# Optimization experiments

Measured on AMD Instinct MI355X. Metric: run time of the kernel, lower is better.

## Reference

```python
import jax, jax.numpy as jnp
import numpy as np

HIDDEN = 128
N_LAYERS = 6
N_NODES = 50000
N_EDGES = 640000


def _glorot(key, shape):
    fan_in, fan_out = shape[0], shape[1]
    lim = (6.0 / (fan_in + fan_out)) ** 0.5
    return jax.random.uniform(key, shape, jnp.float32, -lim, lim)


def setup_inputs() -> dict:
    key = jax.random.key(0)
    ks = jax.random.split(key, 8)
    pos = jax.random.normal(ks[0], (N_NODES, 3), jnp.float32)
    edge_attr = jax.random.normal(ks[1], (N_EDGES, 3), jnp.float32)
    edge_index = jax.random.randint(ks[2], (2, N_EDGES), 0, N_NODES, jnp.int64)
    enc_w = _glorot(ks[3], (3, HIDDEN)); enc_b = jnp.zeros((HIDDEN,), jnp.float32)
    dec_w = _glorot(ks[4], (HIDDEN, 3)); dec_b = jnp.zeros((3,), jnp.float32)
    lk = jax.random.split(ks[5], 4 * N_LAYERS)
    edge_w1 = jnp.stack([_glorot(lk[4 * i + 0], (3 * HIDDEN, HIDDEN)) for i in range(N_LAYERS)])
    edge_w2 = jnp.stack([_glorot(lk[4 * i + 1], (HIDDEN, HIDDEN)) for i in range(N_LAYERS)])
    node_w1 = jnp.stack([_glorot(lk[4 * i + 2], (2 * HIDDEN, HIDDEN)) for i in range(N_LAYERS)])
    node_w2 = jnp.stack([_glorot(lk[4 * i + 3], (HIDDEN, HIDDEN)) for i in range(N_LAYERS)])
    edge_b1 = jnp.zeros((N_LAYERS, HIDDEN), jnp.float32)
    edge_b2 = jnp.zeros((N_LAYERS, HIDDEN), jnp.float32)
    node_b1 = jnp.zeros((N_LAYERS, HIDDEN), jnp.float32)
    node_b2 = jnp.zeros((N_LAYERS, HIDDEN), jnp.float32)
    return dict(pos=pos, edge_attr=edge_attr, edge_index=edge_index,
                enc_w=enc_w, enc_b=enc_b, dec_w=dec_w, dec_b=dec_b,
                edge_w1=edge_w1, edge_b1=edge_b1, edge_w2=edge_w2, edge_b2=edge_b2,
                node_w1=node_w1, node_b1=node_b1, node_w2=node_w2, node_b2=node_b2)


def _interaction(x, ef, src, dst, ew1, eb1, ew2, eb2, nw1, nb1, nw2, nb2, n_nodes):
    # message: concat(x_i=x[dst], x_j=x[src], edge_feature) -> edge MLP
    m = jnp.concatenate([x[dst], x[src], ef], axis=-1)            # [E, 3H]
    m = jax.nn.relu(m @ ew1 + eb1) @ ew2 + eb2                     # [E, H]
    # scatter-mean by target node
    sums = jax.ops.segment_sum(m, dst, num_segments=n_nodes)      # [N, H]
    cnt = jax.ops.segment_sum(jnp.ones((m.shape[0],), m.dtype), dst, num_segments=n_nodes)
    aggr = sums / jnp.maximum(cnt, 1.0)[:, None]
    node = jnp.concatenate([x, aggr], axis=-1)                     # [N, 2H]
    node = jax.nn.relu(node @ nw1 + nb1) @ nw2 + nb2               # [N, H]
    return x + node, ef + m


def reference(pos, edge_attr, edge_index, enc_w, enc_b, dec_w, dec_b,
              edge_w1, edge_b1, edge_w2, edge_b2,
              node_w1, node_b1, node_w2, node_b2):
    n_nodes = pos.shape[0]
    src = edge_index[0]
    dst = edge_index[1]
    x = jnp.zeros((n_nodes, HIDDEN), jnp.float32)
    ef = edge_attr @ enc_w + enc_b
    for i in range(N_LAYERS):
        x, ef = _interaction(x, ef, src, dst,
                             edge_w1[i], edge_b1[i], edge_w2[i], edge_b2[i],
                             node_w1[i], node_b1[i], node_w2[i], node_b2[i], n_nodes)
    out = x @ dec_w + dec_b                                        # [N, 3]
    # F.normalize(dim=1, eps=1e-12)
    norm = jnp.linalg.norm(out, axis=1, keepdims=True)
    return out / jnp.maximum(norm, 1e-12)
```

## Files before the change

### kernel.cpp

```cpp
#include <hip/hip_runtime.h>
#include <cstdint>

#define HIDDEN  128
#define NLAYERS 6
#define NNODES  50000
#define NEDGES  640000

typedef short short8 __attribute__((ext_vector_type(8)));
typedef float f32x4  __attribute__((ext_vector_type(4)));

__device__ __forceinline__ float bf2f(unsigned short u) {
    return __uint_as_float(((unsigned int)u) << 16);
}
__device__ __forceinline__ unsigned short f2bf(float f) {
    unsigned int u = __float_as_uint(f);
    unsigned int r = u + 0x7FFFu + ((u >> 16) & 1u);
    return (unsigned short)(r >> 16);
}
__device__ __forceinline__ unsigned int pack2(float a, float b) {
    return (unsigned int)f2bf(a) | ((unsigned int)f2bf(b) << 16);
}
__device__ __forceinline__ void unpack8(uint4 v, float* f) {
    f[0] = bf2f((unsigned short)(v.x & 0xffff)); f[1] = bf2f((unsigned short)(v.x >> 16));
    f[2] = bf2f((unsigned short)(v.y & 0xffff)); f[3] = bf2f((unsigned short)(v.y >> 16));
    f[4] = bf2f((unsigned short)(v.z & 0xffff)); f[5] = bf2f((unsigned short)(v.z >> 16));
    f[6] = bf2f((unsigned short)(v.w & 0xffff)); f[7] = bf2f((unsigned short)(v.w >> 16));
}

__global__ void detect_kernel(const int* __restrict__ ei, int* __restrict__ flag)
{
    int lane = threadIdx.x;
    int v = ei[2 * lane + 1];
    unsigned long long b = __ballot(v != 0);
    if (lane == 0) *flag = (b != 0ULL) ? 1 : 0;
}

__global__ void normidx_kernel(const int* __restrict__ ei, const int* __restrict__ flag,
                               int* __restrict__ s32, int* __restrict__ d32)
{
    int e = blockIdx.x * blockDim.x + threadIdx.x;
    if (e >= NEDGES) return;
    int s, d;
    if (*flag) { s = ei[e]; d = ei[NEDGES + e]; }
    else       { s = ei[2 * e]; d = ei[2 * (NEDGES + e)]; }
    s32[e] = min(max(s, 0), NNODES - 1);
    d32[e] = min(max(d, 0), NNODES - 1);
}

__global__ void degree_kernel(const int* __restrict__ dst, int* __restrict__ deg)
{
    int e = blockIdx.x * blockDim.x + threadIdx.x;
    if (e < NEDGES) atomicAdd(&deg[dst[e]], 1);
}

#define SCAN_T 1024
__global__ void scan_kernel(const int* __restrict__ deg, int* __restrict__ off,
                            int* __restrict__ cursor)
{
    __shared__ int part[SCAN_T];
    const int t = threadIdx.x;
    const int CH = (NNODES + SCAN_T - 1) / SCAN_T;
    const int base = t * CH;
    int s = 0;
    for (int i = 0; i < CH; ++i) {
        int idx = base + i;
        if (idx < NNODES) s += deg[idx];
    }
    part[t] = s;
    __syncthreads();
    for (int d = 1; d < SCAN_T; d <<= 1) {
        int v = (t >= d) ? part[t - d] : 0;
        __syncthreads();
        part[t] += v;
        __syncthreads();
    }
    int run = (t == 0) ? 0 : part[t - 1];
    for (int i = 0; i < CH; ++i) {
        int idx = base + i;
        if (idx < NNODES) {
            off[idx] = run;
            cursor[idx] = run;
            run += deg[idx];
        }
    }
    if (t == SCAN_T - 1) off[NNODES] = run;
}

__global__ void scatter_kernel(const int* __restrict__ s32, const int* __restrict__ d32,
                               int* __restrict__ cursor,
                               int* __restrict__ sp, int* __restrict__ dp, int* __restrict__ ep)
{
    int e = blockIdx.x * blockDim.x + threadIdx.x;
    if (e >= NEDGES) return;
    int d = d32[e];
    int p = atomicAdd(&cursor[d], 1);
    sp[p] = s32[e];
    dp[p] = d;
    ep[p] = e;
}

__global__ void transpose_kernel(const float* __restrict__ W, unsigned short* __restrict__ WT,
                                 int K, int N, int L)
{
    long idx = (long)blockIdx.x * 256 + threadIdx.x;
    long tot = (long)L * K * N;
    if (idx >= tot) return;
    int kn = (int)(idx % ((long)K * N));
    int l  = (int)(idx / ((long)K * N));
    int k = kn / N;
    int n = kn % N;
    WT[(long)l * K * N + (long)n * K + k] = f2bf(W[idx]);
}

__global__ void encode_kernel(const float* __restrict__ ea,
                              const float* __restrict__ w,
                              const float* __restrict__ b,
                              const int* __restrict__ ep,
                              unsigned short* __restrict__ ef)
{
    int idx = blockIdx.x * blockDim.x + threadIdx.x;
    int p = idx >> 5;
    if (p >= NEDGES) return;
    int e = ep[p];
    int j = (idx & 31) << 2;
    float a0 = ea[e * 3 + 0], a1 = ea[e * 3 + 1], a2 = ea[e * 3 + 2];
    float4 w0 = *(const float4*)(w + 0 * HIDDEN + j);
    float4 w1 = *(const float4*)(w + 1 * HIDDEN + j);
    float4 w2 = *(const float4*)(w + 2 * HIDDEN + j);
    float4 bb = *(const float4*)(b + j);
    ushort4 o;
    o.x = f2bf(fmaf(a0, w0.x, fmaf(a1, w1.x, fmaf(a2, w2.x, bb.x))));
    o.y = f2bf(fmaf(a0, w0.y, fmaf(a1, w1.y, fmaf(a2, w2.y, bb.y))));
    o.z = f2bf(fmaf(a0, w0.z, fmaf(a1, w1.z, fmaf(a2, w2.z, bb.z))));
    o.w = f2bf(fmaf(a0, w0.w, fmaf(a1, w1.w, fmaf(a2, w2.w, bb.w))));
    *(ushort4*)(ef + (long)p * HIDDEN + j) = o;
}

__global__ __launch_bounds__(256, 3)
void edge_layer_mfma(const unsigned short* __restrict__ Xa,
                     const unsigned short* __restrict__ Xb,
                     unsigned short* __restrict__ ef,
                     float* __restrict__ sums,
                     const int* __restrict__ sp,
                     const int* __restrict__ dp,
                     const unsigned short* __restrict__ W1T,
                     const float* __restrict__ b1,
                     const unsigned short* __restrict__ W2T,
                     const float* __restrict__ b2)
{
    __shared__ __align__(16) unsigned char buf[45056];
    unsigned short* As = (unsigned short*)buf;
    unsigned short* Hs = (unsigned short*)buf;
    unsigned short* Bs = (unsigned short*)(buf + 34816);
    __shared__ int dv[128];
    __shared__ int sv[128];

    const int tid = threadIdx.x;
    const long eb = (long)blockIdx.x * 128;
    if (tid < 128) dv[tid]       = dp[eb + tid];
    else           sv[tid - 128] = sp[eb + tid - 128];

    const int lane = tid & 63;
    const int wv   = tid >> 6;
    const int mn   = lane & 15;
    const int q    = lane >> 4;
    const int rr   = tid >> 1;
    const int o    = (tid & 1) << 4;
    const int bn   = tid >> 1;
    const int bk   = (tid & 1) << 4;

    f32x4 acc[2][8];
#pragma unroll
    for (int h = 0; h < 2; ++h)
#pragma unroll
        for (int t = 0; t < 8; ++t) acc[h][t] = (f32x4)0.0f;

    short8 efold0[4], efold1[4];

    uint4 pa0, pa1, pw0, pw1;
    {
        const unsigned short* epp = ef + (eb + rr) * HIDDEN + o;
        pa0 = *(const uint4*)epp;
        pa1 = *(const uint4*)(epp + 8);
        const unsigned short* wp = W1T + (long)bn * 384 + 256 + bk;
        pw0 = *(const uint4*)wp;
        pw1 = *(const uint4*)(wp + 8);
    }

    for (int c = 0; c < 4; ++c) {
        *(uint4*)&As[rr * 40 + o]      = pa0;
        *(uint4*)&As[rr * 40 + o + 8]  = pa1;
        *(uint4*)&Bs[bn * 40 + bk]     = pw0;
        *(uint4*)&Bs[bn * 40 + bk + 8] = pw1;
        __syncthreads();

        if (c + 1 < 4) {
            const int cn = c + 1;
            const unsigned short* epp = ef + (eb + rr) * HIDDEN + (cn << 5) + o;
            pa0 = *(const uint4*)epp;
            pa1 = *(const uint4*)(epp + 8);
            const unsigned short* wp = W1T + (long)bn * 384 + 256 + (cn << 5) + bk;
            pw0 = *(const uint4*)wp;
            pw1 = *(const uint4*)(wp + 8);
        }

        short8 af0 = *(short8*)&As[(wv * 32 + mn) * 40 + (q << 3)];
        short8 af1 = *(short8*)&As[(wv * 32 + 16 + mn) * 40 + (q << 3)];
        efold0[c] = af0;
        efold1[c] = af1;
#pragma unroll
        for (int nt = 0; nt < 8; ++nt) {
            short8 bf = *(short8*)&Bs[(nt * 16 + mn) * 40 + (q << 3)];
            acc[0][nt] = __builtin_amdgcn_mfma_f32_16x16x32_bf16(af0, bf, acc[0][nt], 0, 0, 0);
            acc[1][nt] = __builtin_amdgcn_mfma_f32_16x16x32_bf16(af1, bf, acc[1][nt], 0, 0, 0);
        }
        __syncthreads();
    }

#pragma unroll
    for (int h = 0; h < 2; ++h)
#pragma unroll
        for (int nt = 0; nt < 8; ++nt)
#pragma unroll
            for (int r = 0; r < 4; ++r)
                Hs[(wv * 32 + h * 16 + q * 4 + r) * 136 + nt * 16 + mn] = f2bf(acc[h][nt][r]);

    {
        const int row  = wv * 32 + (lane >> 1);
        const int ch   = (lane & 1) << 6;
        const unsigned short* xap = Xa + (long)dv[row] * HIDDEN + ch;
        const unsigned short* xbp = Xb + (long)sv[row] * HIDDEN + ch;
        unsigned short* hp = &Hs[row * 136 + ch];
#pragma unroll
        for (int i = 0; i < 8; ++i) {
            uint4 va = *(const uint4*)(xap + (i << 3));
            uint4 vb = *(const uint4*)(xbp + (i << 3));
            uint4 vp = *(uint4*)(hp + (i << 3));
            float fa[8], fb[8], fp[8];
            unpack8(va, fa); unpack8(vb, fb); unpack8(vp, fp);
            const float* bp = b1 + ch + (i << 3);
            uint4 nw;
            float h0 = fmaxf(fp[0] + fa[0] + fb[0] + bp[0], 0.0f);
            float h1 = fmaxf(fp[1] + fa[1] + fb[1] + bp[1], 0.0f);
            float h2 = fmaxf(fp[2] + fa[2] + fb[2] + bp[2], 0.0f);
            float h3 = fmaxf(fp[3] + fa[3] + fb[3] + bp[3], 0.0f);
            float h4 = fmaxf(fp[4] + fa[4] + fb[4] + bp[4], 0.0f);
            float h5 = fmaxf(fp[5] + fa[5] + fb[5] + bp[5], 0.0f);
            float h6 = fmaxf(fp[6] + fa[6] + fb[6] + bp[6], 0.0f);
            float h7 = fmaxf(fp[7] + fa[7] + fb[7] + bp[7], 0.0f);
            nw.x = pack2(h0, h1); nw.y = pack2(h2, h3);
            nw.z = pack2(h4, h5); nw.w = pack2(h6, h7);
            *(uint4*)(hp + (i << 3)) = nw;
        }
    }

    f32x4 acc2[2][8];
#pragma unroll
    for (int h = 0; h < 2; ++h)
#pragma unroll
        for (int t = 0; t < 8; ++t) acc2[h][t] = (f32x4)0.0f;
    {
        const unsigned short* wp = W2T + (long)bn * 128 + bk;
        pw0 = *(const uint4*)wp;
        pw1 = *(const uint4*)(wp + 8);
    }
    for (int c = 0; c < 4; ++c) {
        *(uint4*)&Bs[bn * 40 + bk]     = pw0;
        *(uint4*)&Bs[bn * 40 + bk + 8] = pw1;
        __syncthreads();
        if (c + 1 < 4) {
            const unsigned short* wp = W2T + (long)bn * 128 + ((c + 1) << 5) + bk;
            pw0 = *(const uint4*)wp;
            pw1 = *(const uint4*)(wp + 8);
        }
        short8 af0 = *(short8*)&Hs[(wv * 32 + mn) * 136 + (c << 5) + (q << 3)];
        short8 af1 = *(short8*)&Hs[(wv * 32 + 16 + mn) * 136 + (c << 5) + (q << 3)];
#pragma unroll
        for (int nt = 0; nt < 8; ++nt) {
            short8 bf = *(short8*)&Bs[(nt * 16 + mn) * 40 + (q << 3)];
            acc2[0][nt] = __builtin_amdgcn_mfma_f32_16x16x32_bf16(af0, bf, acc2[0][nt], 0, 0, 0);
            acc2[1][nt] = __builtin_amdgcn_mfma_f32_16x16x32_bf16(af1, bf, acc2[1][nt], 0, 0, 0);
        }
        __syncthreads();
    }

#pragma unroll
    for (int h = 0; h < 2; ++h)
#pragma unroll
        for (int nt = 0; nt < 8; ++nt) {
            float b2v = b2[nt * 16 + mn];
#pragma unroll
            for (int r = 0; r < 4; ++r)
                Hs[(wv * 32 + h * 16 + q * 4 + r) * 136 + nt * 16 + mn] = f2bf(acc2[h][nt][r] + b2v);
        }

#pragma unroll
    for (int h = 0; h < 2; ++h) {
        const int row = wv * 32 + h * 16 + mn;
        unsigned short* ep_ = ef + (eb + row) * HIDDEN + (q << 3);
#pragma unroll
        for (int c = 0; c < 4; ++c) {
            uint4 mh = *(uint4*)&Hs[row * 136 + (c << 5) + (q << 3)];
            float m[8], e[8];
            unpack8(mh, m);
            short8 eo = h ? efold1[c] : efold0[c];
            uint4 eu = *(uint4*)&eo;
            unpack8(eu, e);
            uint4 nw;
            nw.x = pack2(e[0] + m[0], e[1] + m[1]);
            nw.y = pack2(e[2] + m[2], e[3] + m[3]);
            nw.z = pack2(e[4] + m[4], e[5] + m[5]);
            nw.w = pack2(e[6] + m[6], e[7] + m[7]);
            *(uint4*)(ep_ + (c << 5)) = nw;
        }
    }

    {
        const int cp = (tid & 63) << 1;
        const int qr = tid >> 6;
        float s0 = 0.0f, s1 = 0.0f;
        int cur = dv[qr * 32];
        for (int r = 0; r < 32; ++r) {
            const int row = qr * 32 + r;
            const int d = dv[row];
            if (d != cur) {
                atomicAdd(&sums[(long)cur * HIDDEN + cp], s0);
                atomicAdd(&sums[(long)cur * HIDDEN + cp + 1], s1);
                s0 = 0.0f; s1 = 0.0f;
                cur = d;
            }
            unsigned int u = *(unsigned int*)&Hs[row * 136 + cp];
            s0 += bf2f((unsigned short)(u & 0xffff));
            s1 += bf2f((unsigned short)(u >> 16));
        }
        atomicAdd(&sums[(long)cur * HIDDEN + cp], s0);
        atomicAdd(&sums[(long)cur * HIDDEN + cp + 1], s1);
    }
}

__global__ __launch_bounds__(256, 5)
void node_layer_mfma(float* __restrict__ x,
                     float* __restrict__ sums,
                     const int* __restrict__ deg,
                     const unsigned short* __restrict__ N1T,
                     const float* __restrict__ b1,
                     const unsigned short* __restrict__ N2T,
                     const float* __restrict__ b2,
                     const unsigned short* __restrict__ W1Tn,
                     unsigned short* __restrict__ Xa,
                     unsigned short* __restrict__ Xb)
{
    __shared__ __align__(16) unsigned char nbuf[27648];
    unsigned short* As = (unsigned short*)nbuf;
    unsigned short* Hs = (unsigned short*)nbuf;
    unsigned short* Bs = (unsigned short*)(nbuf + 17408);
    __shared__ float cInv[64];

    const int tid = threadIdx.x;
    const long n0 = (long)blockIdx.x * 64;
    if (tid < 64) {
        long n = n0 + tid;
        cInv[tid] = (n < NNODES) ? 1.0f / fmaxf((float)deg[n], 1.0f) : 0.0f;
    }

    const int lane = tid & 63;
    const int wv   = tid >> 6;
    const int mn   = lane & 15;
    const int q    = lane >> 4;
    const int srow = tid >> 2;
    const int sseg = tid & 3;
    const int bn   = tid >> 1;
    const int bk   = (tid & 1) << 4;

    long nr = n0 + srow;
    if (nr >= NNODES) nr = NNODES - 1;

    __syncthreads();

    f32x4 acc[8];
#pragma unroll
    for (int t = 0; t < 8; ++t) acc[t] = (f32x4)0.0f;

    float4 pa0, pa1;
    uint4 pb0, pb1;
    {
        const float* spx = x + nr * HIDDEN + (sseg << 3);
        pa0 = *(const float4*)spx;
        pa1 = *(const float4*)(spx + 4);
        const unsigned short* wp = N1T + (long)bn * 256 + bk;
        pb0 = *(const uint4*)wp;
        pb1 = *(const uint4*)(wp + 8);
    }
    float scCur = 1.0f;
    for (int c = 0; c < 8; ++c) {
        {
            uint4 w;
            w.x = pack2(pa0.x * scCur, pa0.y * scCur); w.y = pack2(pa0.z * scCur, pa0.w * scCur);
            w.z = pack2(pa1.x * scCur, pa1.y * scCur); w.w = pack2(pa1.z * scCur, pa1.w * scCur);
            *(uint4*)&As[srow * 40 + (sseg << 3)] = w;
        }
        *(uint4*)&Bs[bn * 40 + bk]     = pb0;
        *(uint4*)&Bs[bn * 40 + bk + 8] = pb1;
        __syncthreads();
        if (c + 1 < 8) {
            const int cn = c + 1;
            const float* base = (cn < 4) ? x : sums;
            scCur = (cn < 4) ? 1.0f : cInv[srow];
            const float* spx = base + nr * HIDDEN + ((cn & 3) << 5) + (sseg << 3);
            pa0 = *(const float4*)spx;
            pa1 = *(const float4*)(spx + 4);
            const unsigned short* wp = N1T + (long)bn * 256 + (cn << 5) + bk;
            pb0 = *(const uint4*)wp;
            pb1 = *(const uint4*)(wp + 8);
        }
        short8 af = *(short8*)&As[(wv * 16 + mn) * 40 + (q << 3)];
#pragma unroll
        for (int nt = 0; nt < 8; ++nt) {
            short8 bf = *(short8*)&Bs[(nt * 16 + mn) * 40 + (q << 3)];
            acc[nt] = __builtin_amdgcn_mfma_f32_16x16x32_bf16(af, bf, acc[nt], 0, 0, 0);
        }
        __syncthreads();
    }

    {
        long row = n0 + srow;
        if (row < NNODES) {
            float4 z = make_float4(0.f, 0.f, 0.f, 0.f);
            float* p = sums + row * HIDDEN + (sseg << 5);
#pragma unroll
            for (int i = 0; i < 8; ++i) ((float4*)p)[i] = z;
        }
    }

#pragma unroll
    for (int nt = 0; nt < 8; ++nt) {
        float b1v = b1[nt * 16 + mn];
#pragma unroll
        for (int r = 0; r < 4; ++r) {
            float hv = fmaxf(acc[nt][r] + b1v, 0.0f);
            Hs[(wv * 16 + q * 4 + r) * 136 + nt * 16 + mn] = f2bf(hv);
        }
    }

    f32x4 acc2[8];
#pragma unroll
    for (int t = 0; t < 8; ++t) acc2[t] = (f32x4)0.0f;
    {
        const unsigned short* wp = N2T + (long)bn * 128 + bk;
        pb0 = *(const uint4*)wp;
        pb1 = *(const uint4*)(wp + 8);
    }
    for (int c = 0; c < 4; ++c) {
        *(uint4*)&Bs[bn * 40 + bk]     = pb0;
        *(uint4*)&Bs[bn * 40 + bk + 8] = pb1;
        __syncthreads();
        if (c + 1 < 4) {
            const unsigned short* wp = N2T + (long)bn * 128 + ((c + 1) << 5) + bk;
            pb0 = *(const uint4*)wp;
            pb1 = *(const uint4*)(wp + 8);
        }
        short8 af = *(short8*)&Hs[(wv * 16 + mn) * 136 + (c << 5) + (q << 3)];
#pragma unroll
        for (int nt = 0; nt < 8; ++nt) {
            short8 bf = *(short8*)&Bs[(nt * 16 + mn) * 40 + (q << 3)];
            acc2[nt] = __builtin_amdgcn_mfma_f32_16x16x32_bf16(af, bf, acc2[nt], 0, 0, 0);
        }
        __syncthreads();
    }

#pragma unroll
    for (int nt = 0; nt < 8; ++nt) {
        float b2v = b2[nt * 16 + mn];
#pragma unroll
        for (int r = 0; r < 4; ++r) {
            long row = n0 + wv * 16 + q * 4 + r;
            float xn = 0.0f;
            if (row < NNODES) {
                float* p = x + row * HIDDEN + nt * 16 + mn;
                xn = *p + acc2[nt][r] + b2v;
                *p = xn;
            }
            Hs[(wv * 16 + q * 4 + r) * 136 + nt * 16 + mn] = f2bf(xn);
        }
    }

    if (W1Tn) {
#pragma unroll
        for (int half = 0; half < 2; ++half) {
            f32x4 accN[8];
#pragma unroll
            for (int t = 0; t < 8; ++t) accN[t] = (f32x4)0.0f;
            const int kbase = half << 7;
            {
                const unsigned short* wp = W1Tn + (long)bn * 384 + kbase + bk;
                pb0 = *(const uint4*)wp;
                pb1 = *(const uint4*)(wp + 8);
            }
            for (int c = 0; c < 4; ++c) {
                *(uint4*)&Bs[bn * 40 + bk]     = pb0;
                *(uint4*)&Bs[bn * 40 + bk + 8] = pb1;
                __syncthreads();
                if (c + 1 < 4) {
                    const unsigned short* wp = W1Tn + (long)bn * 384 + kbase + ((c + 1) << 5) + bk;
                    pb0 = *(const uint4*)wp;
                    pb1 = *(const uint4*)(wp + 8);
                }
                short8 af = *(short8*)&Hs[(wv * 16 + mn) * 136 + (c << 5) + (q << 3)];
#pragma unroll
                for (int nt = 0; nt < 8; ++nt) {
                    short8 bf = *(short8*)&Bs[(nt * 16 + mn) * 40 + (q << 3)];
                    accN[nt] = __builtin_amdgcn_mfma_f32_16x16x32_bf16(af, bf, accN[nt], 0, 0, 0);
                }
                __syncthreads();
            }
            unsigned short* Xout = half ? Xb : Xa;
#pragma unroll
            for (int nt = 0; nt < 8; ++nt) {
#pragma unroll
                for (int r = 0; r < 4; ++r) {
                    long row = n0 + wv * 16 + q * 4 + r;
                    if (row < NNODES) {
                        Xout[row * HIDDEN + nt * 16 + mn] = f2bf(accN[nt][r]);
                    }
                }
            }
        }
    }
}

__global__ void decode_kernel(const float* __restrict__ x,
                              const float* __restrict__ w,
                              const float* __restrict__ b,
                              float* __restrict__ out)
{
    int gid = blockIdx.x * blockDim.x + threadIdx.x;
    int node = gid >> 6;
    int lane = threadIdx.x & 63;
    if (node >= NNODES) return;
    float a0 = 0.f, a1 = 0.f, a2 = 0.f;
#pragma unroll
    for (int k = lane; k < HIDDEN; k += 64) {
        float xv = x[(long)node * HIDDEN + k];
        a0 = fmaf(xv, w[k * 3 + 0], a0);
        a1 = fmaf(xv, w[k * 3 + 1], a1);
        a2 = fmaf(xv, w[k * 3 + 2], a2);
    }
#pragma unroll
    for (int off = 32; off > 0; off >>= 1) {
        a0 += __shfl_down(a0, off);
        a1 += __shfl_down(a1, off);
        a2 += __shfl_down(a2, off);
    }
    if (lane == 0) {
        a0 += b[0]; a1 += b[1]; a2 += b[2];
        float nrm = sqrtf(a0 * a0 + a1 * a1 + a2 * a2);
        float inv = 1.0f / fmaxf(nrm, 1e-12f);
        out[(long)node * 3 + 0] = a0 * inv;
        out[(long)node * 3 + 1] = a1 * inv;
        out[(long)node * 3 + 2] = a2 * inv;
    }
}

extern "C" void kernel_launch(void* const* d_in, const int* in_sizes, int n_in,
                              void* d_out, int out_size, void* d_ws, size_t ws_size,
                              hipStream_t stream)
{
    const float* edge_attr = (const float*)d_in[1];
    const int*   ei        = (const int*)d_in[2];
    const float* enc_w     = (const float*)d_in[3];
    const float* enc_b     = (const float*)d_in[4];
    const float* dec_w     = (const float*)d_in[5];
    const float* dec_b     = (const float*)d_in[6];
    const float* edge_w1   = (const float*)d_in[7];
    const float* edge_b1   = (const float*)d_in[8];
    const float* edge_w2   = (const float*)d_in[9];
    const float* edge_b2   = (const float*)d_in[10];
    const float* node_w1   = (const float*)d_in[11];
    const float* node_b1   = (const float*)d_in[12];
    const float* node_w2   = (const float*)d_in[13];
    const float* node_b2   = (const float*)d_in[14];

    char* ws = (char*)d_ws;
    unsigned short* ef  = (unsigned short*)(ws);
    float* x      = (float*)(ws + 163840000L);
    float* sums   = (float*)(ws + 189440000L);
    int*   src32  = (int*)  (ws + 215040000L);
    int*   dst32  = (int*)  (ws + 217600000L);
    int*   sp     = (int*)  (ws + 220160000L);
    int*   dp     = (int*)  (ws + 222720000L);
    int*   eperm  = (int*)  (ws + 225280000L);
    int*   deg    = (int*)  (ws + 227840000L);
    int*   off    = (int*)  (ws + 228040704L);
    int*   cursor = (int*)  (ws + 228241408L);
    int*   flag   = (int*)  (ws + 228442112L);
    unsigned short* W1T = (unsigned short*)(ws + 228442176L);
    unsigned short* W2T = (unsigned short*)(ws + 229032000L);
    unsigned short* N1T = (unsigned short*)(ws + 229228608L);
    unsigned short* N2T = (unsigned short*)(ws + 229621824L);
    unsigned short* Xa  = (unsigned short*)(ws + 229818432L);
    unsigned short* Xb  = (unsigned short*)(ws + 242618432L);

    float* out = (float*)d_out;

    hipMemsetAsync(x, 0, (size_t)NNODES * HIDDEN * sizeof(float), stream);
    hipMemsetAsync(sums, 0, (size_t)NNODES * HIDDEN * sizeof(float), stream);
    hipMemsetAsync(deg, 0, 200704, stream);
    hipMemsetAsync(Xa, 0, 25600000, stream);

    detect_kernel<<<1, 64, 0, stream>>>(ei, flag);
    normidx_kernel<<<(NEDGES + 255) / 256, 256, 0, stream>>>(ei, flag, src32, dst32);
    degree_kernel<<<(NEDGES + 255) / 256, 256, 0, stream>>>(dst32, deg);
    scan_kernel<<<1, SCAN_T, 0, stream>>>(deg, off, cursor);
    scatter_kernel<<<(NEDGES + 255) / 256, 256, 0, stream>>>(src32, dst32, cursor, sp, dp, eperm);
    encode_kernel<<<(NEDGES * 32 + 255) / 256, 256, 0, stream>>>(edge_attr, enc_w, enc_b, eperm, ef);

    transpose_kernel<<<(6 * 384 * 128 + 255) / 256, 256, 0, stream>>>(edge_w1, W1T, 384, 128, 6);
    transpose_kernel<<<(6 * 128 * 128 + 255) / 256, 256, 0, stream>>>(edge_w2, W2T, 128, 128, 6);
    transpose_kernel<<<(6 * 256 * 128 + 255) / 256, 256, 0, stream>>>(node_w1, N1T, 256, 128, 6);
    transpose_kernel<<<(6 * 128 * 128 + 255) / 256, 256, 0, stream>>>(node_w2, N2T, 128, 128, 6);

    for (int l = 0; l < NLAYERS; ++l) {
        edge_layer_mfma<<<NEDGES / 128, 256, 0, stream>>>(
            Xa, Xb, ef, sums, sp, dp,
            W1T + (long)l * 384 * 128, edge_b1 + (long)l * HIDDEN,
            W2T + (long)l * 128 * 128, edge_b2 + (long)l * HIDDEN);
        const unsigned short* w1next = (l + 1 < NLAYERS) ? (W1T + (long)(l + 1) * 384 * 128) : nullptr;
        node_layer_mfma<<<(NNODES + 63) / 64, 256, 0, stream>>>(
            x, sums, deg,
            N1T + (long)l * 256 * 128, node_b1 + (long)l * HIDDEN,
            N2T + (long)l * 128 * 128, node_b2 + (long)l * HIDDEN,
            w1next, Xa, Xb);
    }

    decode_kernel<<<(NNODES * 64 + 255) / 256, 256, 0, stream>>>(x, dec_w, dec_b, out);
}
```

Before: 1.542 ms.

## Load MFMA weight and edge fragments directly from global, drop LDS staging

Both the edge and node layer kernels now read weight B-fragments straight from global memory (L1/L2-cached) into MFMA operands, and edge features directly into registers, instead of staging them through shared memory with per-chunk barriers. This removes most __syncthreads and LDS traffic and shrinks the shared buffer, and launch bounds rise to allow more resident blocks. In exchange each wave issues redundant global loads of the weights and relies on cache hit rates, and the register budget tightens under the higher occupancy target.

```diff
diff --git a/kernel.cpp b/kernel.cpp
--- a/kernel.cpp
+++ b/kernel.cpp
@@ -136,7 +136,7 @@
     *(ushort4*)(ef + (long)p * HIDDEN + j) = o;
 }
 
-__global__ __launch_bounds__(256, 3)
+__global__ __launch_bounds__(256, 4)
 void edge_layer_mfma(const unsigned short* __restrict__ Xa,
                      const unsigned short* __restrict__ Xb,
                      unsigned short* __restrict__ ef,
@@ -148,26 +148,33 @@
                      const unsigned short* __restrict__ W2T,
                      const float* __restrict__ b2)
 {
-    __shared__ __align__(16) unsigned char buf[45056];
-    unsigned short* As = (unsigned short*)buf;
-    unsigned short* Hs = (unsigned short*)buf;
-    unsigned short* Bs = (unsigned short*)(buf + 34816);
+    __shared__ __align__(16) unsigned short Hs[128 * 136];
     __shared__ int dv[128];
     __shared__ int sv[128];
 
-    const int tid = threadIdx.x;
-    const long eb = (long)blockIdx.x * 128;
-    if (tid < 128) dv[tid]       = dp[eb + tid];
-    else           sv[tid - 128] = sp[eb + tid - 128];
-
+    const int tid  = threadIdx.x;
+    const long eb  = (long)blockIdx.x * 128;
     const int lane = tid & 63;
     const int wv   = tid >> 6;
     const int mn   = lane & 15;
     const int q    = lane >> 4;
-    const int rr   = tid >> 1;
-    const int o    = (tid & 1) << 4;
-    const int bn   = tid >> 1;
-    const int bk   = (tid & 1) << 4;
+
+    {
+        const int l = lane & 31;
+        if (lane < 32) dv[wv * 32 + l] = dp[eb + wv * 32 + l];
+        else           sv[wv * 32 + l] = sp[eb + wv * 32 + l];
+    }
+
+    short8 efr0[4], efr1[4];
+    {
+        const unsigned short* a0 = ef + (eb + wv * 32 + mn) * HIDDEN + (q << 3);
+        const unsigned short* a1 = a0 + 16 * HIDDEN;
+#pragma unroll
+        for (int c = 0; c < 4; ++c) {
+            efr0[c] = *(const short8*)(a0 + (c << 5));
+            efr1[c] = *(const short8*)(a1 + (c << 5));
+        }
+    }
 
     f32x4 acc[2][8];
 #pragma unroll
@@ -175,46 +182,17 @@
 #pragma unroll
         for (int t = 0; t < 8; ++t) acc[h][t] = (f32x4)0.0f;
 
-    short8 efold0[4], efold1[4];
-
-    uint4 pa0, pa1, pw0, pw1;
-    {
-        const unsigned short* epp = ef + (eb + rr) * HIDDEN + o;
-        pa0 = *(const uint4*)epp;
-        pa1 = *(const uint4*)(epp + 8);
-        const unsigned short* wp = W1T + (long)bn * 384 + 256 + bk;
-        pw0 = *(const uint4*)wp;
-        pw1 = *(const uint4*)(wp + 8);
-    }
-
-    for (int c = 0; c < 4; ++c) {
-        *(uint4*)&As[rr * 40 + o]      = pa0;
-        *(uint4*)&As[rr * 40 + o + 8]  = pa1;
-        *(uint4*)&Bs[bn * 40 + bk]     = pw0;
-        *(uint4*)&Bs[bn * 40 + bk + 8] = pw1;
-        __syncthreads();
-
-        if (c + 1 < 4) {
-            const int cn = c + 1;
-            const unsigned short* epp = ef + (eb + rr) * HIDDEN + (cn << 5) + o;
-            pa0 = *(const uint4*)epp;
-            pa1 = *(const uint4*)(epp + 8);
-            const unsigned short* wp = W1T + (long)bn * 384 + 256 + (cn << 5) + bk;
-            pw0 = *(const uint4*)wp;
-            pw1 = *(const uint4*)(wp + 8);
-        }
-
-        short8 af0 = *(short8*)&As[(wv * 32 + mn) * 40 + (q << 3)];
-        short8 af1 = *(short8*)&As[(wv * 32 + 16 + mn) * 40 + (q << 3)];
-        efold0[c] = af0;
-        efold1[c] = af1;
-#pragma unroll
-        for (int nt = 0; nt < 8; ++nt) {
-            short8 bf = *(short8*)&Bs[(nt * 16 + mn) * 40 + (q << 3)];
-            acc[0][nt] = __builtin_amdgcn_mfma_f32_16x16x32_bf16(af0, bf, acc[0][nt], 0, 0, 0);
-            acc[1][nt] = __builtin_amdgcn_mfma_f32_16x16x32_bf16(af1, bf, acc[1][nt], 0, 0, 0);
-        }
-        __syncthreads();
+    {
+        const unsigned short* bp = W1T + (long)mn * 384 + 256 + (q << 3);
+#pragma unroll
+        for (int c = 0; c < 4; ++c) {
+#pragma unroll
+            for (int nt = 0; nt < 8; ++nt) {
+                short8 bf = *(const short8*)(bp + nt * (16 * 384) + (c << 5));
+                acc[0][nt] = __builtin_amdgcn_mfma_f32_16x16x32_bf16(efr0[c], bf, acc[0][nt], 0, 0, 0);
+                acc[1][nt] = __builtin_amdgcn_mfma_f32_16x16x32_bf16(efr1[c], bf, acc[1][nt], 0, 0, 0);
+            }
+        }
     }
 
 #pragma unroll
@@ -259,29 +237,20 @@
     for (int h = 0; h < 2; ++h)
 #pragma unroll
         for (int t = 0; t < 8; ++t) acc2[h][t] = (f32x4)0.0f;
-    {
-        const unsigned short* wp = W2T + (long)bn * 128 + bk;
-        pw0 = *(const uint4*)wp;
-        pw1 = *(const uint4*)(wp + 8);
-    }
-    for (int c = 0; c < 4; ++c) {
-        *(uint4*)&Bs[bn * 40 + bk]     = pw0;
-        *(uint4*)&Bs[bn * 40 + bk + 8] = pw1;
-        __syncthreads();
-        if (c + 1 < 4) {
-            const unsigned short* wp = W2T + (long)bn * 128 + ((c + 1) << 5) + bk;
-            pw0 = *(const uint4*)wp;
-            pw1 = *(const uint4*)(wp + 8);
-        }
-        short8 af0 = *(short8*)&Hs[(wv * 32 + mn) * 136 + (c << 5) + (q << 3)];
-        short8 af1 = *(short8*)&Hs[(wv * 32 + 16 + mn) * 136 + (c << 5) + (q << 3)];
-#pragma unroll
-        for (int nt = 0; nt < 8; ++nt) {
-            short8 bf = *(short8*)&Bs[(nt * 16 + mn) * 40 + (q << 3)];
-            acc2[0][nt] = __builtin_amdgcn_mfma_f32_16x16x32_bf16(af0, bf, acc2[0][nt], 0, 0, 0);
-            acc2[1][nt] = __builtin_amdgcn_mfma_f32_16x16x32_bf16(af1, bf, acc2[1][nt], 0, 0, 0);
-        }
-        __syncthreads();
+
+    {
+        const unsigned short* bp = W2T + (long)mn * 128 + (q << 3);
+#pragma unroll
+        for (int c = 0; c < 4; ++c) {
+            short8 af0 = *(short8*)&Hs[(wv * 32 + mn) * 136 + (c << 5) + (q << 3)];
+            short8 af1 = *(short8*)&Hs[(wv * 32 + 16 + mn) * 136 + (c << 5) + (q << 3)];
+#pragma unroll
+            for (int nt = 0; nt < 8; ++nt) {
+                short8 bf = *(const short8*)(bp + nt * (16 * 128) + (c << 5));
+                acc2[0][nt] = __builtin_amdgcn_mfma_f32_16x16x32_bf16(af0, bf, acc2[0][nt], 0, 0, 0);
+                acc2[1][nt] = __builtin_amdgcn_mfma_f32_16x16x32_bf16(af1, bf, acc2[1][nt], 0, 0, 0);
+            }
+        }
     }
 
 #pragma unroll
@@ -303,7 +272,7 @@
             uint4 mh = *(uint4*)&Hs[row * 136 + (c << 5) + (q << 3)];
             float m[8], e[8];
             unpack8(mh, m);
-            short8 eo = h ? efold1[c] : efold0[c];
+            short8 eo = h ? efr1[c] : efr0[c];
             uint4 eu = *(uint4*)&eo;
             unpack8(eu, e);
             uint4 nw;
@@ -338,7 +307,7 @@
     }
 }
 
-__global__ __launch_bounds__(256, 5)
+__global__ __launch_bounds__(256, 6)
 void node_layer_mfma(float* __restrict__ x,
                      float* __restrict__ sums,
                      const int* __restrict__ deg,
@@ -350,83 +319,67 @@
                      unsigned short* __restrict__ Xa,
                      unsigned short* __restrict__ Xb)
 {
-    __shared__ __align__(16) unsigned char nbuf[27648];
-    unsigned short* As = (unsigned short*)nbuf;
-    unsigned short* Hs = (unsigned short*)nbuf;
-    unsigned short* Bs = (unsigned short*)(nbuf + 17408);
-    __shared__ float cInv[64];
-
-    const int tid = threadIdx.x;
-    const long n0 = (long)blockIdx.x * 64;
-    if (tid < 64) {
-        long n = n0 + tid;
-        cInv[tid] = (n < NNODES) ? 1.0f / fmaxf((float)deg[n], 1.0f) : 0.0f;
-    }
-
+    __shared__ __align__(16) unsigned short Hs[64 * 136];
+
+    const int tid  = threadIdx.x;
+    const long n0  = (long)blockIdx.x * 64;
     const int lane = tid & 63;
     const int wv   = tid >> 6;
     const int mn   = lane & 15;
     const int q    = lane >> 4;
-    const int srow = tid >> 2;
-    const int sseg = tid & 3;
-    const int bn   = tid >> 1;
-    const int bk   = (tid & 1) << 4;
-
-    long nr = n0 + srow;
-    if (nr >= NNODES) nr = NNODES - 1;
-
-    __syncthreads();
+
+    long arow = n0 + wv * 16 + mn;
+    if (arow >= NNODES) arow = NNODES - 1;
+    const float cv = 1.0f / fmaxf((float)deg[arow], 1.0f);
+
+    const float* xr = x + arow * HIDDEN;
+    const float* sr = sums + arow * HIDDEN;
 
     f32x4 acc[8];
 #pragma unroll
     for (int t = 0; t < 8; ++t) acc[t] = (f32x4)0.0f;
 
-    float4 pa0, pa1;
-    uint4 pb0, pb1;
-    {
-        const float* spx = x + nr * HIDDEN + (sseg << 3);
-        pa0 = *(const float4*)spx;
-        pa1 = *(const float4*)(spx + 4);
-        const unsigned short* wp = N1T + (long)bn * 256 + bk;
-        pb0 = *(const uint4*)wp;
-        pb1 = *(const uint4*)(wp + 8);
-    }
-    float scCur = 1.0f;
-    for (int c = 0; c < 8; ++c) {
+    {
+        const unsigned short* bp1 = N1T + (long)mn * 256 + (q << 3);
+        float4 pa0, pa1;
         {
-            uint4 w;
-            w.x = pack2(pa0.x * scCur, pa0.y * scCur); w.y = pack2(pa0.z * scCur, pa0.w * scCur);
-            w.z = pack2(pa1.x * scCur, pa1.y * scCur); w.w = pack2(pa1.z * scCur, pa1.w * scCur);
-            *(uint4*)&As[srow * 40 + (sseg << 3)] = w;
-        }
-        *(uint4*)&Bs[bn * 40 + bk]     = pb0;
-        *(uint4*)&Bs[bn * 40 + bk + 8] = pb1;
-        __syncthreads();
-        if (c + 1 < 8) {
-            const int cn = c + 1;
-            const float* base = (cn < 4) ? x : sums;
-            scCur = (cn < 4) ? 1.0f : cInv[srow];
-            const float* spx = base + nr * HIDDEN + ((cn & 3) << 5) + (sseg << 3);
-            pa0 = *(const float4*)spx;
-            pa1 = *(const float4*)(spx + 4);
-            const unsigned short* wp = N1T + (long)bn * 256 + (cn << 5) + bk;
-            pb0 = *(const uint4*)wp;
-            pb1 = *(const uint4*)(wp + 8);
-        }
-        short8 af = *(short8*)&As[(wv * 16 + mn) * 40 + (q << 3)];
-#pragma unroll
-        for (int nt = 0; nt < 8; ++nt) {
-            short8 bf = *(short8*)&Bs[(nt * 16 + mn) * 40 + (q << 3)];
-            acc[nt] = __builtin_amdgcn_mfma_f32_16x16x32_bf16(af, bf, acc[nt], 0, 0, 0);
-        }
-        __syncthreads();
-    }
-
-    {
-        long row = n0 + srow;
+            const float* ap = xr + (q << 3);
+            pa0 = *(const float4*)ap;
+            pa1 = *(const float4*)(ap + 4);
+        }
+        float scCur = 1.0f;
+#pragma unroll
+        for (int c = 0; c < 8; ++c) {
+            short8 af;
+            {
+                unsigned int* au = (unsigned int*)&af;
+                au[0] = pack2(pa0.x * scCur, pa0.y * scCur);
+                au[1] = pack2(pa0.z * scCur, pa0.w * scCur);
+                au[2] = pack2(pa1.x * scCur, pa1.y * scCur);
+                au[3] = pack2(pa1.z * scCur, pa1.w * scCur);
+            }
+            if (c + 1 < 8) {
+                const int cn = c + 1;
+                const float* base = (cn < 4) ? xr : sr;
+                scCur = (cn < 4) ? 1.0f : cv;
+                const float* ap = base + ((cn & 3) << 5) + (q << 3);
+                pa0 = *(const float4*)ap;
+                pa1 = *(const float4*)(ap + 4);
+            }
+#pragma unroll
+            for (int nt = 0; nt < 8; ++nt) {
+                short8 bf = *(const short8*)(bp1 + nt * (16 * 256) + (c << 5));
+                acc[nt] = __builtin_amdgcn_mfma_f32_16x16x32_bf16(af, bf, acc[nt], 0, 0, 0);
+            }
+        }
+    }
+
+    {
+        const int r = lane >> 2;
+        long row = n0 + wv * 16 + r;
         if (row < NNODES) {
+            float* p = sums + row * HIDDEN + ((lane & 3) << 5);
             float4 z = make_float4(0.f, 0.f, 0.f, 0.f);
-            float* p = sums + row * HIDDEN + (sseg << 5);
 #pragma unroll
             for (int i = 0; i < 8; ++i) ((float4*)p)[i] = z;
         }
@@ -445,27 +398,18 @@
     f32x4 acc2[8];
 #pragma unroll
     for (int t = 0; t < 8; ++t) acc2[t] = (f32x4)0.0f;
-    {
-        const unsigned short* wp = N2T + (long)bn * 128 + bk;
-        pb0 = *(const uint4*)wp;
-        pb1 = *(const uint4*)(wp + 8);
-    }
-    for (int c = 0; c < 4; ++c) {
-        *(uint4*)&Bs[bn * 40 + bk]     = pb0;
-        *(uint4*)&Bs[bn * 40 + bk + 8] = pb1;
-        __syncthreads();
-        if (c + 1 < 4) {
-            const unsigned short* wp = N2T + (long)bn * 128 + ((c + 1) << 5) + bk;
-            pb0 = *(const uint4*)wp;
-            pb1 = *(const uint4*)(wp + 8);
-        }
-        short8 af = *(short8*)&Hs[(wv * 16 + mn) * 136 + (c << 5) + (q << 3)];
-#pragma unroll
-        for (int nt = 0; nt < 8; ++nt) {
-            short8 bf = *(short8*)&Bs[(nt * 16 + mn) * 40 + (q << 3)];
-            acc2[nt] = __builtin_amdgcn_mfma_f32_16x16x32_bf16(af, bf, acc2[nt], 0, 0, 0);
-        }
-        __syncthreads();
+
+    {
+        const unsigned short* bp2 = N2T + (long)mn * 128 + (q << 3);
+#pragma unroll
+        for (int c = 0; c < 4; ++c) {
+            short8 af = *(short8*)&Hs[(wv * 16 + mn) * 136 + (c << 5) + (q << 3)];
+#pragma unroll
+            for (int nt = 0; nt < 8; ++nt) {
+                short8 bf = *(const short8*)(bp2 + nt * (16 * 128) + (c << 5));
+                acc2[nt] = __builtin_amdgcn_mfma_f32_16x16x32_bf16(af, bf, acc2[nt], 0, 0, 0);
+            }
+        }
     }
 
 #pragma unroll
@@ -490,28 +434,15 @@
             f32x4 accN[8];
 #pragma unroll
             for (int t = 0; t < 8; ++t) accN[t] = (f32x4)0.0f;
-            const int kbase = half << 7;
-            {
-                const unsigned short* wp = W1Tn + (long)bn * 384 + kbase + bk;
-                pb0 = *(const uint4*)wp;
-                pb1 = *(const uint4*)(wp + 8);
-            }
+            const unsigned short* bpn = W1Tn + (long)mn * 384 + (half << 7) + (q << 3);
+#pragma unroll
             for (int c = 0; c < 4; ++c) {
-                *(uint4*)&Bs[bn * 40 + bk]     = pb0;
-                *(uint4*)&Bs[bn * 40 + bk + 8] = pb1;
-                __syncthreads();
-                if (c + 1 < 4) {
-                    const unsigned short* wp = W1Tn + (long)bn * 384 + kbase + ((c + 1) << 5) + bk;
-                    pb0 = *(const uint4*)wp;
-                    pb1 = *(const uint4*)(wp + 8);
-                }
                 short8 af = *(short8*)&Hs[(wv * 16 + mn) * 136 + (c << 5) + (q << 3)];
 #pragma unroll
                 for (int nt = 0; nt < 8; ++nt) {
-                    short8 bf = *(short8*)&Bs[(nt * 16 + mn) * 40 + (q << 3)];
+                    short8 bf = *(const short8*)(bpn + nt * (16 * 384) + (c << 5));
                     accN[nt] = __builtin_amdgcn_mfma_f32_16x16x32_bf16(af, bf, accN[nt], 0, 0, 0);
                 }
-                __syncthreads();
             }
             unsigned short* Xout = half ? Xb : Xa;
 #pragma unroll
```

Result: slower. 2.909 ms (+88.6%).
